# Kernel optimization log

Measured on AMD Instinct MI355X. Metric: run time of the kernel, lower is better.

The kernel has to match this reference:

```python
import jax, jax.numpy as jnp
import numpy as np

B, L, H = 64, 512, 768

def setup_inputs() -> dict:
    key = jax.random.key(0)
    k1, k2, k3, k4 = jax.random.split(key, 4)
    scale = 1.0 / np.sqrt(H)
    return {
        "hidden_states": jax.random.normal(k1, (B, L, H), dtype=jnp.float32),
        "W_fc": jax.random.normal(k2, (H, H), dtype=jnp.float32) * scale,
        "b_fc": jax.random.normal(k3, (H,), dtype=jnp.float32) * scale,
        "W_nu": jax.random.normal(k4, (H,), dtype=jnp.float32) * scale,
    }

def reference(hidden_states, W_fc, b_fc, W_nu):
    # upsilon = tanh(Linear(hidden_states)); [B, L, H]
    upsilon = jnp.tanh(jnp.einsum("blh,hk->blk", hidden_states, W_fc.T) + b_fc)
    # per-token attention logits: [B, L]  (replaces per-sample torch.mv loop)
    nu = jnp.einsum("blh,h->bl", upsilon, W_nu)
    alphas = jax.nn.softmax(nu, axis=1)
    # weighted-sum pooling: [B, H]  (replaces per-sample torch.mm loop)
    pooled = jnp.einsum("bl,blh->bh", alphas, hidden_states)
    return pooled
```

## Files before the change

kernel.cpp:

```cpp
#include <hip/hip_runtime.h>

#define H_DIM 768
#define B_DIM 64
#define L_DIM 512
#define M_TOT (B_DIM*L_DIM)
#define BM 128
#define BN 128
#define BK 64
#define NB_CNT (H_DIM/BN)
#define KB_CNT (H_DIM/BK)
#define MB_CNT (M_TOT/BM)
#define TILE_HALFS (BM*BK)

#define GBM 256
#define GMB_CNT (M_TOT/GBM)
#define BUF_HALFS 24576
#define B_OFF 16384

typedef _Float16 f16x8 __attribute__((ext_vector_type(8)));
typedef float f32x4 __attribute__((ext_vector_type(4)));

#define WS_W16   0u
#define WS_NUP   1179648u
#define WS_ALPHA 1966080u
#define WS_POOL  2097152u
#define WS_AIMG  3670016u
#define WS_NEED_IMG (WS_AIMG + (size_t)M_TOT*H_DIM*2)

__device__ __forceinline__ void gload_lds16(const void* g, void* l) {
  __builtin_amdgcn_global_load_lds((const __attribute__((address_space(1))) void*)g,
                                   (__attribute__((address_space(3))) void*)l, 16, 0, 0);
}

__device__ __forceinline__ f16x8 cvt8(const float* src) {
  f32x4 x0 = *(const f32x4*)src;
  f32x4 x1 = *(const f32x4*)(src + 4);
  f16x8 h;
  h[0]=(_Float16)x0[0]; h[1]=(_Float16)x0[1]; h[2]=(_Float16)x0[2]; h[3]=(_Float16)x0[3];
  h[4]=(_Float16)x1[0]; h[5]=(_Float16)x1[1]; h[6]=(_Float16)x1[2]; h[7]=(_Float16)x1[3];
  return h;
}

__device__ __forceinline__ float fast_tanh(float v) {
  float e = __builtin_amdgcn_exp2f(v * 2.8853900817779268f);
  return 1.0f - 2.0f * __builtin_amdgcn_rcpf(e + 1.0f);
}

#define SBAR()  do { __builtin_amdgcn_sched_barrier(0); \
                     __builtin_amdgcn_s_barrier(); \
                     __builtin_amdgcn_sched_barrier(0); } while (0)

__global__ __launch_bounds__(256) void wconv_kernel(const float* __restrict__ Wfc,
                                                    _Float16* __restrict__ W16) {
  int t = blockIdx.x;
  int nb = t / KB_CNT, kb = t % KB_CNT;
  for (int i = 0; i < 4; ++i) {
    int u = threadIdx.x + i * 256;
    int row = u >> 3, sp = u & 7;
    int sl = sp ^ (row & 7);
    *(f16x8*)(W16 + (size_t)t*TILE_HALFS + u*8) =
        cvt8(Wfc + (size_t)(nb*BN + row)*H_DIM + kb*BK + sl*8);
  }
}

__global__ __launch_bounds__(256) void aconv_kernel(const float* __restrict__ A,
                                                    _Float16* __restrict__ img) {
  int t = blockIdx.x;
  int mb = t / KB_CNT, kb = t % KB_CNT;
  _Float16* tile = img + (size_t)t * TILE_HALFS;
  for (int i = 0; i < 4; ++i) {
    int u = threadIdx.x + i * 256;
    int row = u >> 3, sp = u & 7;
    int sl = sp ^ (row & 7);
    *(f16x8*)(tile + u*8) =
        cvt8(A + (size_t)(mb*BM + row)*H_DIM + kb*BK + sl*8);
  }
}

__device__ __forceinline__ void stage256(const _Float16* a0, const _Float16* a1,
                                         const _Float16* wt, _Float16* Lb, int tid) {
  gload_lds16(a0 + tid*8,          Lb + tid*8);
  gload_lds16(a0 + (tid+512)*8,    Lb + (tid+512)*8);
  gload_lds16(a1 + tid*8,          Lb + 8192 + tid*8);
  gload_lds16(a1 + (tid+512)*8,    Lb + 8192 + (tid+512)*8);
  gload_lds16(wt + tid*8,          Lb + B_OFF + tid*8);
  gload_lds16(wt + (tid+512)*8,    Lb + B_OFF + (tid+512)*8);
}

__device__ __forceinline__ void rd_frags(const _Float16* base, const int aoff[4],
                                         const int boff[4], int slot,
                                         f16x8 af[4], f16x8 bf[4]) {
#pragma unroll
  for (int mi = 0; mi < 4; ++mi) af[mi] = *(const f16x8*)(base + aoff[mi] + slot);
#pragma unroll
  for (int ni = 0; ni < 4; ++ni) bf[ni] = *(const f16x8*)(base + boff[ni] + slot);
}

__device__ __forceinline__ void mfma16(const f16x8 af[4], const f16x8 bf[4],
                                       f32x4 acc[4][4]) {
  __builtin_amdgcn_s_setprio(1);
#pragma unroll
  for (int mi = 0; mi < 4; ++mi)
#pragma unroll
    for (int ni = 0; ni < 4; ++ni)
      acc[mi][ni] = __builtin_amdgcn_mfma_f32_16x16x32_f16(af[mi], bf[ni], acc[mi][ni], 0, 0, 0);
  __builtin_amdgcn_s_setprio(0);
}

__global__ __launch_bounds__(512, 2) void gemm_nu_img_kernel(const _Float16* __restrict__ Aimg,
                                                             const _Float16* __restrict__ W16,
                                                             const float* __restrict__ bfc,
                                                             const float* __restrict__ wnu,
                                                             float* __restrict__ nup) {
  __shared__ __align__(16) _Float16 LS[2 * BUF_HALFS];
  __shared__ float nred[2][GBM];

  int bid = blockIdx.x;
  int mb = bid & (GMB_CNT - 1);
  int nb = bid >> 7;
  int m0 = mb * GBM, n0 = nb * BN;
  int tid = threadIdx.x;
  int wv = tid >> 6, ln = tid & 63;
  int wr = wv >> 1, wc = wv & 1;
  int lrow = ln & 15, lk = ln >> 4;

  f32x4 acc[4][4] = {};
  f16x8 af0[4], bf0[4], af1[4], bf1[4];
  const _Float16* a0b = Aimg + (size_t)((2*mb)   * KB_CNT) * TILE_HALFS;
  const _Float16* a1b = Aimg + (size_t)((2*mb+1) * KB_CNT) * TILE_HALFS;
  const _Float16* wtb = W16  + (size_t)(nb * KB_CNT) * TILE_HALFS;
  _Float16* b0 = LS;
  _Float16* b1 = LS + BUF_HALFS;

  int aoff[4], boff[4];
#pragma unroll
  for (int mi = 0; mi < 4; ++mi) {
    int r = wr*64 + mi*16 + lrow;
    aoff[mi] = (r>>7)*8192 + (r&127)*64;
  }
#pragma unroll
  for (int ni = 0; ni < 4; ++ni) {
    int rb = wc*64 + ni*16 + lrow;
    boff[ni] = B_OFF + rb*64;
  }
  int slot0 = ((0*4 + lk) ^ (lrow & 7)) * 8;
  int slot1 = ((1*4 + lk) ^ (lrow & 7)) * 8;

  float wn[4], bb[4];
#pragma unroll
  for (int ni = 0; ni < 4; ++ni) {
    int c = n0 + wc*64 + ni*16 + lrow;
    wn[ni] = wnu[c];
    bb[ni] = bfc[c];
  }
  asm volatile("" :: "v"(wn[0]), "v"(wn[1]), "v"(wn[2]), "v"(wn[3]),
                     "v"(bb[0]), "v"(bb[1]), "v"(bb[2]), "v"(bb[3]));
  asm volatile("s_waitcnt vmcnt(0)" ::: "memory");

  stage256(a0b,        a1b,        wtb,        b0, tid);
  stage256(a0b + 8192, a1b + 8192, wtb + 8192, b1, tid);
  asm volatile("s_waitcnt vmcnt(6)" ::: "memory");
  SBAR();
  rd_frags(b0, aoff, boff, slot0, af0, bf0);

#pragma unroll 1
  for (int kt2 = 0; kt2 < 5; ++kt2) {
    size_t k2 = (size_t)(kt2*2 + 2) * 8192;
    size_t k3 = (size_t)(kt2*2 + 3) * 8192;
    rd_frags(b0, aoff, boff, slot1, af1, bf1);
    mfma16(af0, bf0, acc);
    asm volatile("s_waitcnt lgkmcnt(0)" ::: "memory");
    SBAR();
    stage256(a0b + k2, a1b + k2, wtb + k2, b0, tid);
    asm volatile("s_waitcnt vmcnt(6)" ::: "memory");
    SBAR();
    rd_frags(b1, aoff, boff, slot0, af0, bf0);
    mfma16(af1, bf1, acc);
    rd_frags(b1, aoff, boff, slot1, af1, bf1);
    mfma16(af0, bf0, acc);
    asm volatile("s_waitcnt lgkmcnt(0)" ::: "memory");
    SBAR();
    stage256(a0b + k3, a1b + k3, wtb + k3, b1, tid);
    asm volatile("s_waitcnt vmcnt(6)" ::: "memory");
    SBAR();
    rd_frags(b0, aoff, boff, slot0, af0, bf0);
    mfma16(af1, bf1, acc);
  }

  rd_frags(b0, aoff, boff, slot1, af1, bf1);
  mfma16(af0, bf0, acc);
  asm volatile("s_waitcnt vmcnt(0)" ::: "memory");
  SBAR();
  rd_frags(b1, aoff, boff, slot0, af0, bf0);
  mfma16(af1, bf1, acc);
  rd_frags(b1, aoff, boff, slot1, af1, bf1);
  mfma16(af0, bf0, acc);
  mfma16(af1, bf1, acc);

#pragma unroll
  for (int mi = 0; mi < 4; ++mi) {
#pragma unroll
    for (int r = 0; r < 4; ++r) {
      float s = 0.f;
#pragma unroll
      for (int ni = 0; ni < 4; ++ni)
        s = fmaf(fast_tanh(acc[mi][ni][r] + bb[ni]), wn[ni], s);
      for (int o = 1; o < 16; o <<= 1) s += __shfl_xor(s, o, 64);
      if (lrow == 0) nred[wc][wr*64 + mi*16 + lk*4 + r] = s;
    }
  }
  __syncthreads();
  if (tid < GBM)
    nup[(size_t)nb * M_TOT + m0 + tid] = nred[0][tid] + nred[1][tid];
}

__global__ __launch_bounds__(256) void gemm_nu_kernel(const float* __restrict__ A,
                                                      const _Float16* __restrict__ W16,
                                                      const float* __restrict__ bfc,
                                                      const float* __restrict__ wnu,
                                                      float* __restrict__ nup) {
  __shared__ __align__(16) _Float16 lsA[TILE_HALFS];
  __shared__ __align__(16) _Float16 lsB[TILE_HALFS];
  __shared__ float nred[2][BM];

  int bid = blockIdx.x;
  int nb = bid % NB_CNT;
  int mb = bid / NB_CNT;
  int m0 = mb * BM, n0 = nb * BN;
  int tid = threadIdx.x;
  int wv = tid >> 6, ln = tid & 63;
  int wr = wv >> 1, wc = wv & 1;
  int lrow = ln & 15, lk = ln >> 4;

  f32x4 acc[4][4] = {};
  const _Float16* wbase = W16 + (size_t)(nb * KB_CNT) * TILE_HALFS;

  for (int kb = 0; kb < KB_CNT; ++kb) {
    const _Float16* wt = wbase + (size_t)kb * TILE_HALFS;
    for (int i = 0; i < 4; ++i) {
      int e = i*2048 + wv*512 + ln*8;
      gload_lds16(wt + e, lsB + e);
    }
    for (int i = 0; i < 4; ++i) {
      int u = tid + i * 256;
      int row = u >> 3, sl = u & 7;
      *(f16x8*)(lsA + row*BK + ((sl ^ (row & 7)) * 8)) =
          cvt8(A + (size_t)(m0 + row) * H_DIM + kb*BK + sl*8);
    }
    __syncthreads();
#pragma unroll
    for (int kk = 0; kk < 2; ++kk) {
      f16x8 af[4], bf[4];
      int s = kk*4 + lk;
#pragma unroll
      for (int mi = 0; mi < 4; ++mi) {
        int r = wr*64 + mi*16 + lrow;
        af[mi] = *(const f16x8*)(lsA + r*BK + ((s ^ (r & 7)) * 8));
      }
#pragma unroll
      for (int ni = 0; ni < 4; ++ni) {
        int r = wc*64 + ni*16 + lrow;
        bf[ni] = *(const f16x8*)(lsB + r*BK + ((s ^ (r & 7)) * 8));
      }
#pragma unroll
      for (int mi = 0; mi < 4; ++mi)
#pragma unroll
        for (int ni = 0; ni < 4; ++ni)
          acc[mi][ni] = __builtin_amdgcn_mfma_f32_16x16x32_f16(af[mi], bf[ni], acc[mi][ni], 0, 0, 0);
    }
    __syncthreads();
  }

  float wn[4], bb[4];
  for (int ni = 0; ni < 4; ++ni) {
    int c = n0 + wc*64 + ni*16 + lrow;
    wn[ni] = wnu[c];
    bb[ni] = bfc[c];
  }
  for (int mi = 0; mi < 4; ++mi) {
    for (int r = 0; r < 4; ++r) {
      float s = 0.f;
      for (int ni = 0; ni < 4; ++ni)
        s = fmaf(fast_tanh(acc[mi][ni][r] + bb[ni]), wn[ni], s);
      for (int o = 1; o < 16; o <<= 1) s += __shfl_xor(s, o, 64);
      if (lrow == 0) nred[wc][wr*64 + mi*16 + lk*4 + r] = s;
    }
  }
  __syncthreads();
  if (tid < BM)
    nup[(size_t)nb * M_TOT + m0 + tid] = nred[0][tid] + nred[1][tid];
}

__global__ __launch_bounds__(512) void softmax_kernel(const float* __restrict__ nup,
                                                      float* __restrict__ alphas) {
  int b = blockIdx.x;
  int l = threadIdx.x;
  int m = b * L_DIM + l;
  float v = 0.f;
  for (int nb = 0; nb < NB_CNT; ++nb) v += nup[(size_t)nb * M_TOT + m];
  __shared__ float smax[8], ssum[8];
  int w = l >> 6, ln = l & 63;
  float mx = v;
  for (int o = 1; o < 64; o <<= 1) mx = fmaxf(mx, __shfl_xor(mx, o, 64));
  if (ln == 0) smax[w] = mx;
  __syncthreads();
  mx = smax[0];
  for (int i = 1; i < 8; ++i) mx = fmaxf(mx, smax[i]);
  float e = __expf(v - mx);
  float sm = e;
  for (int o = 1; o < 64; o <<= 1) sm += __shfl_xor(sm, o, 64);
  if (ln == 0) ssum[w] = sm;
  __syncthreads();
  float tot = 0.f;
  for (int i = 0; i < 8; ++i) tot += ssum[i];
  alphas[m] = e / tot;
}

__global__ __launch_bounds__(192) void pool1_img_kernel(const _Float16* __restrict__ img,
                                                        const float* __restrict__ alphas,
                                                        float* __restrict__ part) {
  int b = blockIdx.x >> 3;
  int lc = blockIdx.x & 7;
  int tid = threadIdx.x;
  int g = tid % 96, rp = tid / 96;
  int kb = g >> 3, sl = g & 7;
  __shared__ float al[64];
  __shared__ float tmp[2][H_DIM];
  if (tid < 64) al[tid] = alphas[b * L_DIM + lc*64 + tid];
  __syncthreads();
  float s[8] = {};
  for (int l = rp; l < 64; l += 2) {
    int m = b * L_DIM + lc*64 + l;
    int mb = m >> 7, row = m & 127;
    const f16x8* src = (const f16x8*)(img + ((size_t)(mb*KB_CNT + kb))*TILE_HALFS
                                      + row*64 + ((sl ^ (row & 7)) * 8));
    f16x8 h = *src;
    float a = al[l];
#pragma unroll
    for (int j = 0; j < 8; ++j) s[j] = fmaf(a, (float)h[j], s[j]);
  }
#pragma unroll
  for (int j = 0; j < 8; ++j) tmp[rp][g*8 + j] = s[j];
  __syncthreads();
  float* dst = part + ((size_t)lc * B_DIM + b) * H_DIM + tid*4;
  f32x4 o;
#pragma unroll
  for (int q = 0; q < 4; ++q) o[q] = tmp[0][tid*4 + q] + tmp[1][tid*4 + q];
  *(f32x4*)dst = o;
}

__global__ __launch_bounds__(256) void pool1_kernel(const float* __restrict__ hs,
                                                    const float* __restrict__ alphas,
                                                    float* __restrict__ part) {
  int b = blockIdx.x >> 3;
  int lc = blockIdx.x & 7;
  int tid = threadIdx.x;
  __shared__ float al[64];
  if (tid < 64) al[tid] = alphas[b * L_DIM + lc*64 + tid];
  __syncthreads();
  const float* xp = hs + ((size_t)b * L_DIM + lc*64) * H_DIM;
  int h0 = tid * 3;
  float s0 = 0.f, s1 = 0.f, s2 = 0.f;
  for (int l = 0; l < 64; ++l) {
    float a = al[l];
    const float* r = xp + (size_t)l * H_DIM + h0;
    s0 += a * r[0]; s1 += a * r[1]; s2 += a * r[2];
  }
  float* dst = part + ((size_t)lc * B_DIM + b) * H_DIM + h0;
  dst[0] = s0; dst[1] = s1; dst[2] = s2;
}

__global__ __launch_bounds__(256) void pool2_kernel(const float* __restrict__ part,
                                                    float* __restrict__ out) {
  int i = blockIdx.x * 256 + threadIdx.x;
  float s = 0.f;
  for (int lc = 0; lc < 8; ++lc) s += part[(size_t)lc * (B_DIM * H_DIM) + i];
  out[i] = s;
}

extern "C" void kernel_launch(void* const* d_in, const int* in_sizes, int n_in,
                              void* d_out, int out_size, void* d_ws, size_t ws_size,
                              hipStream_t stream) {
  const float* hs  = (const float*)d_in[0];
  const float* Wfc = (const float*)d_in[1];
  const float* bfc = (const float*)d_in[2];
  const float* wnu = (const float*)d_in[3];
  float* out = (float*)d_out;
  char* ws = (char*)d_ws;
  _Float16* W16 = (_Float16*)(ws + WS_W16);
  float* nup    = (float*)(ws + WS_NUP);
  float* alphas = (float*)(ws + WS_ALPHA);
  float* part   = (float*)(ws + WS_POOL);

  wconv_kernel<<<NB_CNT * KB_CNT, 256, 0, stream>>>(Wfc, W16);
  bool img = (ws_size >= WS_NEED_IMG);
  _Float16* Aimg = (_Float16*)(ws + WS_AIMG);
  if (img) {
    aconv_kernel<<<MB_CNT * KB_CNT, 256, 0, stream>>>(hs, Aimg);
    gemm_nu_img_kernel<<<GMB_CNT * NB_CNT, 512, 0, stream>>>(Aimg, W16, bfc, wnu, nup);
  } else {
    gemm_nu_kernel<<<MB_CNT * NB_CNT, 256, 0, stream>>>(hs, W16, bfc, wnu, nup);
  }
  softmax_kernel<<<B_DIM, 512, 0, stream>>>(nup, alphas);
  if (img) {
    pool1_img_kernel<<<B_DIM * 8, 192, 0, stream>>>(Aimg, alphas, part);
  } else {
    pool1_kernel<<<B_DIM * 8, 256, 0, stream>>>(hs, alphas, part);
  }
  pool2_kernel<<<192, 256, 0, stream>>>(part, out);
}
```

Measured before the change: 103.5 us.

## Shrink GEMM tile to 128x128 with 256 threads and merge conversion kernels

The fused GEMM+nu kernel moves from a 256x128 tile with 512 threads to a 128x128 tile with 256 threads. This doubles the block count and halves LDS per block, aiming for better occupancy and load balance at the cost of more W reloads per output. The separate W and activation fp16 conversion kernels are merged into one launch to save a kernel launch and its tail.

```diff
diff --git a/kernel.cpp b/kernel.cpp
--- a/kernel.cpp
+++ b/kernel.cpp
@@ -11,11 +11,7 @@
 #define KB_CNT (H_DIM/BK)
 #define MB_CNT (M_TOT/BM)
 #define TILE_HALFS (BM*BK)
-
-#define GBM 256
-#define GMB_CNT (M_TOT/GBM)
-#define BUF_HALFS 24576
-#define B_OFF 16384
+#define BUFH 16384
 
 typedef _Float16 f16x8 __attribute__((ext_vector_type(8)));
 typedef float f32x4 __attribute__((ext_vector_type(4)));
@@ -50,41 +46,44 @@
                      __builtin_amdgcn_s_barrier(); \
                      __builtin_amdgcn_sched_barrier(0); } while (0)
 
-__global__ __launch_bounds__(256) void wconv_kernel(const float* __restrict__ Wfc,
-                                                    _Float16* __restrict__ W16) {
+__global__ __launch_bounds__(256) void conv_kernel(const float* __restrict__ Wfc,
+                                                   const float* __restrict__ hs,
+                                                   _Float16* __restrict__ W16,
+                                                   _Float16* __restrict__ Aimg) {
   int t = blockIdx.x;
-  int nb = t / KB_CNT, kb = t % KB_CNT;
+  const float* srcb;
+  _Float16* dstb;
+  if (t < NB_CNT * KB_CNT) {
+    int nb = t / KB_CNT, kb = t % KB_CNT;
+    srcb = Wfc + (size_t)(nb*BN)*H_DIM + kb*BK;
+    dstb = W16 + (size_t)t*TILE_HALFS;
+  } else {
+    int u = t - NB_CNT * KB_CNT;
+    int mb = u / KB_CNT, kb = u % KB_CNT;
+    srcb = hs + (size_t)(mb*BM)*H_DIM + kb*BK;
+    dstb = Aimg + (size_t)u*TILE_HALFS;
+  }
+#pragma unroll
   for (int i = 0; i < 4; ++i) {
     int u = threadIdx.x + i * 256;
     int row = u >> 3, sp = u & 7;
     int sl = sp ^ (row & 7);
-    *(f16x8*)(W16 + (size_t)t*TILE_HALFS + u*8) =
-        cvt8(Wfc + (size_t)(nb*BN + row)*H_DIM + kb*BK + sl*8);
-  }
-}
-
-__global__ __launch_bounds__(256) void aconv_kernel(const float* __restrict__ A,
-                                                    _Float16* __restrict__ img) {
-  int t = blockIdx.x;
-  int mb = t / KB_CNT, kb = t % KB_CNT;
-  _Float16* tile = img + (size_t)t * TILE_HALFS;
+    *(f16x8*)(dstb + u*8) = cvt8(srcb + (size_t)row*H_DIM + sl*8);
+  }
+}
+
+__device__ __forceinline__ void stage128(const _Float16* at, const _Float16* wt,
+                                         _Float16* Lb, int tid) {
+#pragma unroll
   for (int i = 0; i < 4; ++i) {
-    int u = threadIdx.x + i * 256;
-    int row = u >> 3, sp = u & 7;
-    int sl = sp ^ (row & 7);
-    *(f16x8*)(tile + u*8) =
-        cvt8(A + (size_t)(mb*BM + row)*H_DIM + kb*BK + sl*8);
-  }
-}
-
-__device__ __forceinline__ void stage256(const _Float16* a0, const _Float16* a1,
-                                         const _Float16* wt, _Float16* Lb, int tid) {
-  gload_lds16(a0 + tid*8,          Lb + tid*8);
-  gload_lds16(a0 + (tid+512)*8,    Lb + (tid+512)*8);
-  gload_lds16(a1 + tid*8,          Lb + 8192 + tid*8);
-  gload_lds16(a1 + (tid+512)*8,    Lb + 8192 + (tid+512)*8);
-  gload_lds16(wt + tid*8,          Lb + B_OFF + tid*8);
-  gload_lds16(wt + (tid+512)*8,    Lb + B_OFF + (tid+512)*8);
+    int e = (tid + i*256) * 8;
+    gload_lds16(at + e, Lb + e);
+  }
+#pragma unroll
+  for (int i = 0; i < 4; ++i) {
+    int e = (tid + i*256) * 8;
+    gload_lds16(wt + e, Lb + 8192 + e);
+  }
 }
 
 __device__ __forceinline__ void rd_frags(const _Float16* base, const int aoff[4],
@@ -107,18 +106,18 @@
   __builtin_amdgcn_s_setprio(0);
 }
 
-__global__ __launch_bounds__(512, 2) void gemm_nu_img_kernel(const _Float16* __restrict__ Aimg,
+__global__ __launch_bounds__(256, 2) void gemm_nu_img_kernel(const _Float16* __restrict__ Aimg,
                                                              const _Float16* __restrict__ W16,
                                                              const float* __restrict__ bfc,
                                                              const float* __restrict__ wnu,
                                                              float* __restrict__ nup) {
-  __shared__ __align__(16) _Float16 LS[2 * BUF_HALFS];
-  __shared__ float nred[2][GBM];
+  __shared__ __align__(16) _Float16 LS[2 * BUFH];
+  __shared__ float nred[2][BM];
 
   int bid = blockIdx.x;
-  int mb = bid & (GMB_CNT - 1);
-  int nb = bid >> 7;
-  int m0 = mb * GBM, n0 = nb * BN;
+  int mb = bid & (MB_CNT - 1);
+  int nb = bid >> 8;
+  int m0 = mb * BM, n0 = nb * BN;
   int tid = threadIdx.x;
   int wv = tid >> 6, ln = tid & 63;
   int wr = wv >> 1, wc = wv & 1;
@@ -126,23 +125,16 @@
 
   f32x4 acc[4][4] = {};
   f16x8 af0[4], bf0[4], af1[4], bf1[4];
-  const _Float16* a0b = Aimg + (size_t)((2*mb)   * KB_CNT) * TILE_HALFS;
-  const _Float16* a1b = Aimg + (size_t)((2*mb+1) * KB_CNT) * TILE_HALFS;
-  const _Float16* wtb = W16  + (size_t)(nb * KB_CNT) * TILE_HALFS;
+  const _Float16* abase = Aimg + (size_t)(mb * KB_CNT) * TILE_HALFS;
+  const _Float16* wbase = W16  + (size_t)(nb * KB_CNT) * TILE_HALFS;
   _Float16* b0 = LS;
-  _Float16* b1 = LS + BUF_HALFS;
+  _Float16* b1 = LS + BUFH;
 
   int aoff[4], boff[4];
 #pragma unroll
-  for (int mi = 0; mi < 4; ++mi) {
-    int r = wr*64 + mi*16 + lrow;
-    aoff[mi] = (r>>7)*8192 + (r&127)*64;
-  }
-#pragma unroll
-  for (int ni = 0; ni < 4; ++ni) {
-    int rb = wc*64 + ni*16 + lrow;
-    boff[ni] = B_OFF + rb*64;
-  }
+  for (int mi = 0; mi < 4; ++mi) aoff[mi] = (wr*64 + mi*16 + lrow) * 64;
+#pragma unroll
+  for (int ni = 0; ni < 4; ++ni) boff[ni] = 8192 + (wc*64 + ni*16 + lrow) * 64;
   int slot0 = ((0*4 + lk) ^ (lrow & 7)) * 8;
   int slot1 = ((1*4 + lk) ^ (lrow & 7)) * 8;
 
@@ -157,22 +149,24 @@
                      "v"(bb[0]), "v"(bb[1]), "v"(bb[2]), "v"(bb[3]));
   asm volatile("s_waitcnt vmcnt(0)" ::: "memory");
 
-  stage256(a0b,        a1b,        wtb,        b0, tid);
-  stage256(a0b + 8192, a1b + 8192, wtb + 8192, b1, tid);
-  asm volatile("s_waitcnt vmcnt(6)" ::: "memory");
+  stage128(abase,              wbase,              b0, tid);
+  stage128(abase + TILE_HALFS, wbase + TILE_HALFS, b1, tid);
+  asm volatile("s_waitcnt vmcnt(8)" ::: "memory");
   SBAR();
   rd_frags(b0, aoff, boff, slot0, af0, bf0);
 
 #pragma unroll 1
   for (int kt2 = 0; kt2 < 5; ++kt2) {
-    size_t k2 = (size_t)(kt2*2 + 2) * 8192;
-    size_t k3 = (size_t)(kt2*2 + 3) * 8192;
+    const _Float16* a2 = abase + (size_t)(kt2*2 + 2) * TILE_HALFS;
+    const _Float16* w2 = wbase + (size_t)(kt2*2 + 2) * TILE_HALFS;
+    const _Float16* a3 = abase + (size_t)(kt2*2 + 3) * TILE_HALFS;
+    const _Float16* w3 = wbase + (size_t)(kt2*2 + 3) * TILE_HALFS;
     rd_frags(b0, aoff, boff, slot1, af1, bf1);
     mfma16(af0, bf0, acc);
     asm volatile("s_waitcnt lgkmcnt(0)" ::: "memory");
     SBAR();
-    stage256(a0b + k2, a1b + k2, wtb + k2, b0, tid);
-    asm volatile("s_waitcnt vmcnt(6)" ::: "memory");
+    stage128(a2, w2, b0, tid);
+    asm volatile("s_waitcnt vmcnt(8)" ::: "memory");
     SBAR();
     rd_frags(b1, aoff, boff, slot0, af0, bf0);
     mfma16(af1, bf1, acc);
@@ -180,8 +174,8 @@
     mfma16(af0, bf0, acc);
     asm volatile("s_waitcnt lgkmcnt(0)" ::: "memory");
     SBAR();
-    stage256(a0b + k3, a1b + k3, wtb + k3, b1, tid);
-    asm volatile("s_waitcnt vmcnt(6)" ::: "memory");
+    stage128(a3, w3, b1, tid);
+    asm volatile("s_waitcnt vmcnt(8)" ::: "memory");
     SBAR();
     rd_frags(b0, aoff, boff, slot0, af0, bf0);
     mfma16(af1, bf1, acc);
@@ -210,7 +204,7 @@
     }
   }
   __syncthreads();
-  if (tid < GBM)
+  if (tid < BM)
     nup[(size_t)nb * M_TOT + m0 + tid] = nred[0][tid] + nred[1][tid];
 }
 
@@ -238,7 +232,7 @@
   for (int kb = 0; kb < KB_CNT; ++kb) {
     const _Float16* wt = wbase + (size_t)kb * TILE_HALFS;
     for (int i = 0; i < 4; ++i) {
-      int e = i*2048 + wv*512 + ln*8;
+      int e = (tid + i*256) * 8;
       gload_lds16(wt + e, lsB + e);
     }
     for (int i = 0; i < 4; ++i) {
@@ -392,13 +386,13 @@
   float* alphas = (float*)(ws + WS_ALPHA);
   float* part   = (float*)(ws + WS_POOL);
 
-  wconv_kernel<<<NB_CNT * KB_CNT, 256, 0, stream>>>(Wfc, W16);
   bool img = (ws_size >= WS_NEED_IMG);
   _Float16* Aimg = (_Float16*)(ws + WS_AIMG);
   if (img) {
-    aconv_kernel<<<MB_CNT * KB_CNT, 256, 0, stream>>>(hs, Aimg);
-    gemm_nu_img_kernel<<<GMB_CNT * NB_CNT, 512, 0, stream>>>(Aimg, W16, bfc, wnu, nup);
+    conv_kernel<<<(NB_CNT + MB_CNT) * KB_CNT, 256, 0, stream>>>(Wfc, hs, W16, Aimg);
+    gemm_nu_img_kernel<<<MB_CNT * NB_CNT, 256, 0, stream>>>(Aimg, W16, bfc, wnu, nup);
   } else {
+    conv_kernel<<<NB_CNT * KB_CNT, 256, 0, stream>>>(Wfc, hs, W16, Aimg);
     gemm_nu_kernel<<<MB_CNT * NB_CNT, 256, 0, stream>>>(hs, W16, bfc, wnu, nup);
   }
   softmax_kernel<<<B_DIM, 512, 0, stream>>>(nup, alphas);
```

Result: faster. 98.52 us (-4.8%).
